# Optimization experiments

Measured on AMD Instinct MI355X. Metric: run time of the kernel, lower is better.

The kernel has to match this reference:

```python
import jax, jax.numpy as jnp
import numpy as np

N_NODES = 100000
N_EDGES = 1600000
D = 128  # num_node_features == hidden
N_LAYERS = 4


def setup_inputs() -> dict:
    key = jax.random.key(0)
    ks = jax.random.split(key, 6)
    x = jax.random.normal(ks[0], (N_NODES, D), dtype=jnp.float32)
    edge_index = jax.random.randint(ks[1], (2, N_EDGES), 0, N_NODES, dtype=jnp.int32)
    s = 1.0 / np.sqrt(D)
    Wl = jax.random.uniform(ks[2], (N_LAYERS, D, D), jnp.float32, -s, s)
    bl = jax.random.uniform(ks[3], (N_LAYERS, D), jnp.float32, -s, s)
    Wr = jax.random.uniform(ks[4], (N_LAYERS, D, D), jnp.float32, -s, s)
    return {"x": x, "edge_index": edge_index, "Wl": Wl, "bl": bl, "Wr": Wr}


def reference(x, edge_index, Wl, bl, Wr):
    src, dst = edge_index[0], edge_index[1]
    n = x.shape[0]
    # degree of each destination node (clamped to 1, matching scatter_mean)
    deg = jax.ops.segment_sum(jnp.ones_like(dst, dtype=x.dtype), dst, num_segments=n)
    inv_deg = (1.0 / jnp.maximum(deg, 1.0))[:, None]  # [N,1]
    for l in range(Wl.shape[0]):
        # mean-aggregate source features into destination nodes
        agg = jax.ops.segment_sum(x[src], dst, num_segments=n) * inv_deg  # [N,D]
        # SAGEConv: lin_l(agg) + lin_r(x)  (lin_r has no bias), then ReLU
        x = jax.nn.relu(agg @ Wl[l].T + bl[l] + x @ Wr[l].T)
    return x
```

## Files before the change

kernel.cpp:

```cpp
#include <hip/hip_runtime.h>
#include <hip/hip_fp16.h>

#define D 128
#define TM 32
#define AHP 264

typedef float f4v __attribute__((ext_vector_type(4)));
typedef float f2v __attribute__((ext_vector_type(2)));
typedef _Float16 h8v __attribute__((ext_vector_type(8)));

#define Q8_SCALE 16.0f
#define Q8_INV   0.0625f

static __device__ __forceinline__ unsigned pkh(float a, float b) {
    __half2 h = __float22half2_rn(make_float2(a, b));
    return *(unsigned*)&h;
}


__global__ void hist_kernel(const int* __restrict__ dst, int* __restrict__ deg, int E) {
    int i = blockIdx.x * blockDim.x + threadIdx.x;
    if (i < E) atomicAdd(&deg[dst[i]], 1);
}

__global__ void scan1_kernel(const int* __restrict__ deg, int* __restrict__ local_excl,
                             int* __restrict__ blocksum, int n) {
    __shared__ int tmp[1024];
    int i = blockIdx.x * 1024 + threadIdx.x;
    int v = (i < n) ? deg[i] : 0;
    tmp[threadIdx.x] = v;
    __syncthreads();
    for (int off = 1; off < 1024; off <<= 1) {
        int t = 0;
        if (threadIdx.x >= off) t = tmp[threadIdx.x - off];
        __syncthreads();
        if (threadIdx.x >= off) tmp[threadIdx.x] += t;
        __syncthreads();
    }
    int incl = tmp[threadIdx.x];
    if (i < n) local_excl[i] = incl - v;
    if (threadIdx.x == 1023) blocksum[blockIdx.x] = tmp[1023];
}

__global__ void scan2_kernel(int* __restrict__ blocksum, int nb) {
    __shared__ int tmp[1024];
    int v = (threadIdx.x < nb) ? blocksum[threadIdx.x] : 0;
    tmp[threadIdx.x] = v;
    __syncthreads();
    for (int off = 1; off < 1024; off <<= 1) {
        int t = 0;
        if (threadIdx.x >= off) t = tmp[threadIdx.x - off];
        __syncthreads();
        if (threadIdx.x >= off) tmp[threadIdx.x] += t;
        __syncthreads();
    }
    if (threadIdx.x < nb) blocksum[threadIdx.x] = tmp[threadIdx.x] - v;
}

__global__ void scan3_kernel(const int* __restrict__ deg, const int* __restrict__ local_excl,
                             const int* __restrict__ blocksum, int* __restrict__ row_start,
                             int* __restrict__ cursor, float* __restrict__ inv_deg,
                             int n, int n_edges) {
    int i = blockIdx.x * 1024 + threadIdx.x;
    if (i < n) {
        int rs = local_excl[i] + blocksum[blockIdx.x];
        row_start[i] = rs;
        cursor[i]    = rs;
        inv_deg[i]   = 1.0f / fmaxf((float)deg[i], 1.0f);
    }
    if (i == 0) row_start[n] = n_edges;
}

__global__ void scatter_kernel(const int* __restrict__ src, const int* __restrict__ dst,
                               int* __restrict__ cursor, int* __restrict__ csr,
                               int E, int npx) {
    int x  = blockIdx.x & 7;
    int lo = x * npx, hi = lo + npx;
    int stride = (gridDim.x >> 3) * blockDim.x;
    for (int i = (blockIdx.x >> 3) * blockDim.x + threadIdx.x; i < E; i += stride) {
        int d = dst[i];
        if (d >= lo && d < hi) {
            int p = atomicAdd(&cursor[d], 1);
            csr[p] = src[i] << 7;
        }
    }
}

__global__ void prepack_w(const float* __restrict__ Wl, const float* __restrict__ Wr,
                          __half* __restrict__ wpack, int total) {
    int t = blockIdx.x * blockDim.x + threadIdx.x;
    if (t >= total) return;
    int lane = t & 63;
    int ks   = (t >> 6) & 7;
    int ft   = (t >> 9) & 7;
    int l    = t >> 12;
    int f = ft * 16 + (lane & 15);
    int k = (ks & 3) * 32 + ((lane >> 4) << 3);
    const float* W = (ks < 4) ? Wl : Wr;
    const float* src = W + ((size_t)l << 14) + ((size_t)f << 7) + k;
    float4 v0 = *(const float4*)src;
    float4 v1 = *(const float4*)(src + 4);
    uint4 u = {pkh(v0.x, v0.y), pkh(v0.z, v0.w), pkh(v1.x, v1.y), pkh(v1.z, v1.w)};
    ((uint4*)wpack)[t] = u;
}


__global__ void x_to_fp8(const float* __restrict__ x, unsigned* __restrict__ xq, int total4) {
    int i = blockIdx.x * blockDim.x + threadIdx.x;
    if (i < total4) {
        float4 v = ((const float4*)x)[i];
        unsigned u = 0;
        u = __builtin_amdgcn_cvt_pk_fp8_f32(v.x * Q8_SCALE, v.y * Q8_SCALE, u, false);
        u = __builtin_amdgcn_cvt_pk_fp8_f32(v.z * Q8_SCALE, v.w * Q8_SCALE, u, true);
        xq[i] = u;
    }
}


#define ACC16Q(V) {                                                          \
    f2v a0_ = __builtin_amdgcn_cvt_pk_f32_fp8((int)(V).x, false);            \
    f2v a1_ = __builtin_amdgcn_cvt_pk_f32_fp8((int)(V).x, true);             \
    f2v b0_ = __builtin_amdgcn_cvt_pk_f32_fp8((int)(V).y, false);            \
    f2v b1_ = __builtin_amdgcn_cvt_pk_f32_fp8((int)(V).y, true);             \
    f2v c0_ = __builtin_amdgcn_cvt_pk_f32_fp8((int)(V).z, false);            \
    f2v c1_ = __builtin_amdgcn_cvt_pk_f32_fp8((int)(V).z, true);             \
    f2v d0_ = __builtin_amdgcn_cvt_pk_f32_fp8((int)(V).w, false);            \
    f2v d1_ = __builtin_amdgcn_cvt_pk_f32_fp8((int)(V).w, true);             \
    s0.x += a0_.x; s0.y += a0_.y; s0.z += a1_.x; s0.w += a1_.y;              \
    s1.x += b0_.x; s1.y += b0_.y; s1.z += b1_.x; s1.w += b1_.y;              \
    s2.x += c0_.x; s2.y += c0_.y; s2.z += c1_.x; s2.w += c1_.y;              \
    s3.x += d0_.x; s3.y += d0_.y; s3.z += d1_.x; s3.w += d1_.y; }

#define ACC8(V) { const __half2* hp_ = (const __half2*)&(V);                 \
    float2 f0_ = __half22float2(hp_[0]); float2 f1_ = __half22float2(hp_[1]);\
    float2 f2_ = __half22float2(hp_[2]); float2 f3_ = __half22float2(hp_[3]);\
    sA.x += f0_.x; sA.y += f0_.y; sA.z += f1_.x; sA.w += f1_.y;              \
    sB.x += f2_.x; sB.y += f2_.y; sB.z += f3_.x; sB.w += f3_.y; }

template<int INFMT, int OUTFMT>
__global__ __launch_bounds__(256, 4)
void sage_layer_mfma(const float* __restrict__ xin,
                     const void* __restrict__ xq_in,
                     float* __restrict__ xout,
                     void* __restrict__ xq_out,
                     const int* __restrict__ row_start, const int* __restrict__ csr,
                     const float* __restrict__ inv_deg,
                     const __half* __restrict__ wpack,
                     const float* __restrict__ bl, int n_nodes) {
    __shared__ __align__(16) __half Ah[TM][AHP];
    int block0 = blockIdx.x * TM;
    int tid = threadIdx.x;
    int lane = tid & 63;
    int wv   = tid >> 6;

    {
        int row = tid >> 3;
        int seg = tid & 7;
        int nn = block0 + row;
        f4v v0 = {0,0,0,0}, v1 = v0, v2 = v0, v3 = v0;
        if (nn < n_nodes) {
            const f4v* xp = (const f4v*)(xin + (size_t)nn * D) + seg * 4;
            v0 = __builtin_nontemporal_load(xp);
            v1 = __builtin_nontemporal_load(xp + 1);
            v2 = __builtin_nontemporal_load(xp + 2);
            v3 = __builtin_nontemporal_load(xp + 3);
        }
        uint4 ua = {pkh(v0.x,v0.y), pkh(v0.z,v0.w), pkh(v1.x,v1.y), pkh(v1.z,v1.w)};
        uint4 ub = {pkh(v2.x,v2.y), pkh(v2.z,v2.w), pkh(v3.x,v3.y), pkh(v3.z,v3.w)};
        uint4* dst = (uint4*)&Ah[row][128 + seg * 16];
        dst[0] = ua; dst[1] = ub;
    }

    if constexpr (INFMT == 0) {
        int g   = tid >> 3;
        int sub = tid & 7;
        int n = block0 + g;
        float4 s0 = {0,0,0,0}, s1 = {0,0,0,0}, s2 = {0,0,0,0}, s3 = {0,0,0,0};
        float idg = 1.f;
        int e0 = 0, e1 = 0;
        if (n < n_nodes) {
            e0 = row_start[n];
            e1 = row_start[n + 1];
            idg = inv_deg[n];
        }
        int e = e0;
        if (e < e1) {
            int last = e1 - 1;
            const char* qbase = (const char*)xq_in;
            int laneoff = sub * 16;
            int i0 = csr[min(e,     last)];
            int i1 = csr[min(e + 1, last)];
            int i2 = csr[min(e + 2, last)];
            int i3 = csr[min(e + 3, last)];
            while (1) {
                uint4 v0 = *(const uint4*)(qbase + (size_t)(i0 + laneoff));
                uint4 v1 = *(const uint4*)(qbase + (size_t)(i1 + laneoff));
                uint4 v2 = *(const uint4*)(qbase + (size_t)(i2 + laneoff));
                uint4 v3 = *(const uint4*)(qbase + (size_t)(i3 + laneoff));
                int en = e + 4;
                bool more = en < e1;
                int p0, p1, p2, p3;
                if (more) {
                    p0 = csr[min(en,     last)];
                    p1 = csr[min(en + 1, last)];
                    p2 = csr[min(en + 2, last)];
                    p3 = csr[min(en + 3, last)];
                }
                ACC16Q(v0)
                if (e + 1 <= last) ACC16Q(v1)
                if (e + 2 <= last) ACC16Q(v2)
                if (e + 3 <= last) ACC16Q(v3)
                if (!more) break;
                e = en;
                i0 = p0; i1 = p1; i2 = p2; i3 = p3;
            }
        }
        float sc = idg * Q8_INV;
        uint4 ua = {pkh(s0.x*sc,s0.y*sc), pkh(s0.z*sc,s0.w*sc),
                    pkh(s1.x*sc,s1.y*sc), pkh(s1.z*sc,s1.w*sc)};
        uint4 ub = {pkh(s2.x*sc,s2.y*sc), pkh(s2.z*sc,s2.w*sc),
                    pkh(s3.x*sc,s3.y*sc), pkh(s3.z*sc,s3.w*sc)};
        uint4* dst = (uint4*)&Ah[g][sub * 16];
        dst[0] = ua; dst[1] = ub;
    } else {
        int g   = tid >> 4;
        int sub = tid & 15;
        const char* hbase = (const char*)xq_in;
        int laneoff = sub * 16;
        for (int t = 0; t < 2; ++t) {
            int j = g + t * 16;
            int n = block0 + j;
            float4 sA = {0,0,0,0}, sB = {0,0,0,0};
            float idg = 1.f;
            int e0 = 0, e1 = 0;
            if (n < n_nodes) {
                e0 = row_start[n];
                e1 = row_start[n + 1];
                idg = inv_deg[n];
            }
            int e = e0;
            if (e < e1) {
                int last = e1 - 1;
                int i0 = csr[min(e,     last)] << 1;
                int i1 = csr[min(e + 1, last)] << 1;
                int i2 = csr[min(e + 2, last)] << 1;
                int i3 = csr[min(e + 3, last)] << 1;
                while (1) {
                    float4 v0 = *(const float4*)(hbase + (size_t)(i0 + laneoff));
                    float4 v1 = *(const float4*)(hbase + (size_t)(i1 + laneoff));
                    float4 v2 = *(const float4*)(hbase + (size_t)(i2 + laneoff));
                    float4 v3 = *(const float4*)(hbase + (size_t)(i3 + laneoff));
                    int en = e + 4;
                    bool more = en < e1;
                    int p0, p1, p2, p3;
                    if (more) {
                        p0 = csr[min(en,     last)] << 1;
                        p1 = csr[min(en + 1, last)] << 1;
                        p2 = csr[min(en + 2, last)] << 1;
                        p3 = csr[min(en + 3, last)] << 1;
                    }
                    ACC8(v0)
                    if (e + 1 <= last) ACC8(v1)
                    if (e + 2 <= last) ACC8(v2)
                    if (e + 3 <= last) ACC8(v3)
                    if (!more) break;
                    e = en;
                    i0 = p0; i1 = p1; i2 = p2; i3 = p3;
                }
            }
            uint4 u = {pkh(sA.x*idg, sA.y*idg), pkh(sA.z*idg, sA.w*idg),
                       pkh(sB.x*idg, sB.y*idg), pkh(sB.z*idg, sB.w*idg)};
            *(uint4*)&Ah[j][sub * 8] = u;
        }
    }

    uint4 wf[16];
    {
        const uint4* wp = (const uint4*)wpack;
        #pragma unroll
        for (int i = 0; i < 16; ++i) {
            int ft = wv * 2 + (i >> 3);
            int ks = i & 7;
            wf[i] = wp[(size_t)(ft * 8 + ks) * 64 + lane];
        }
    }

    __syncthreads();

    {
        f4v acc[2][2];
        #pragma unroll
        for (int ft = 0; ft < 2; ++ft) {
            int f0 = wv * 32 + ft * 16 + ((lane >> 4) << 2);
            f4v bv = *(const f4v*)(bl + f0);
            acc[ft][0] = bv;
            acc[ft][1] = bv;
        }
        #pragma unroll
        for (int ks = 0; ks < 8; ++ks) {
            int koff = ks * 32 + ((lane >> 4) << 3);
            h8v b0 = *(const h8v*)&Ah[lane & 15][koff];
            h8v b1 = *(const h8v*)&Ah[16 + (lane & 15)][koff];
            h8v a0 = *(const h8v*)&wf[ks];
            h8v a1 = *(const h8v*)&wf[8 + ks];
            acc[0][0] = __builtin_amdgcn_mfma_f32_16x16x32_f16(a0, b0, acc[0][0], 0, 0, 0);
            acc[0][1] = __builtin_amdgcn_mfma_f32_16x16x32_f16(a0, b1, acc[0][1], 0, 0, 0);
            acc[1][0] = __builtin_amdgcn_mfma_f32_16x16x32_f16(a1, b0, acc[1][0], 0, 0, 0);
            acc[1][1] = __builtin_amdgcn_mfma_f32_16x16x32_f16(a1, b1, acc[1][1], 0, 0, 0);
        }
        #pragma unroll
        for (int ft = 0; ft < 2; ++ft) {
            #pragma unroll
            for (int nt = 0; nt < 2; ++nt) {
                int node = block0 + nt * 16 + (lane & 15);
                int f0 = wv * 32 + ft * 16 + ((lane >> 4) << 2);
                f4v r = acc[ft][nt];
                r.x = fmaxf(r.x, 0.f); r.y = fmaxf(r.y, 0.f);
                r.z = fmaxf(r.z, 0.f); r.w = fmaxf(r.w, 0.f);
                if (node < n_nodes) {
                    __builtin_nontemporal_store(r, (f4v*)(xout + (size_t)node * D + f0));
                    if constexpr (OUTFMT == 0) {
                        unsigned u = 0;
                        u = __builtin_amdgcn_cvt_pk_fp8_f32(r.x * Q8_SCALE, r.y * Q8_SCALE, u, false);
                        u = __builtin_amdgcn_cvt_pk_fp8_f32(r.z * Q8_SCALE, r.w * Q8_SCALE, u, true);
                        ((unsigned*)xq_out)[(size_t)node * 32 + (f0 >> 2)] = u;
                    } else if constexpr (OUTFMT == 1) {
                        uint2 u = {pkh(r.x, r.y), pkh(r.z, r.w)};
                        ((uint2*)xq_out)[(size_t)node * 32 + (f0 >> 2)] = u;
                    }
                }
            }
        }
    }
}

extern "C" void kernel_launch(void* const* d_in, const int* in_sizes, int n_in,
                              void* d_out, int out_size, void* d_ws, size_t ws_size,
                              hipStream_t stream) {
    const float* x  = (const float*)d_in[0];
    const int*  edge = (const int*)d_in[1];
    const float* Wl = (const float*)d_in[2];
    const float* bl = (const float*)d_in[3];
    const float* Wr = (const float*)d_in[4];

    int N = in_sizes[0] / D;
    int E = in_sizes[1] / 2;
    int L = in_sizes[3] / D;
    const int* srcp = edge;
    const int* dstp = edge + E;

    char* w = (char*)d_ws;
    auto alloc = [&](size_t bytes) {
        char* p = w;
        w += (bytes + 255) & ~(size_t)255;
        return p;
    };
    int*   deg       = (int*)alloc((size_t)N * 4);
    int*   local_ex  = (int*)alloc((size_t)N * 4);
    int*   row_start = (int*)alloc((size_t)(N + 1) * 4);
    int*   cursor    = (int*)alloc((size_t)N * 4);
    int*   csr       = (int*)alloc((size_t)E * 4);
    float* invdeg    = (float*)alloc((size_t)N * 4);
    int*   blocksum  = (int*)alloc((size_t)1024 * 4);
    __half* wpack    = (__half*)alloc((size_t)L * 32768 * 2);
    float* buf0      = (float*)alloc((size_t)N * D * 4);
    unsigned* q0     = (unsigned*)alloc((size_t)N * D);
    void*  q1        = (void*)alloc((size_t)N * D * 2);

    int nb1 = (N + 1023) / 1024;
    hipMemsetAsync(deg, 0, (size_t)N * 4, stream);
    hist_kernel<<<(E + 255) / 256, 256, 0, stream>>>(dstp, deg, E);
    scan1_kernel<<<nb1, 1024, 0, stream>>>(deg, local_ex, blocksum, N);
    scan2_kernel<<<1, 1024, 0, stream>>>(blocksum, nb1);
    scan3_kernel<<<nb1, 1024, 0, stream>>>(deg, local_ex, blocksum, row_start,
                                           cursor, invdeg, N, E);
    int npx = (N + 7) / 8;
    scatter_kernel<<<2048, 256, 0, stream>>>(srcp, dstp, cursor, csr, E, npx);
    int tp = L * 4096;
    prepack_w<<<(tp + 255) / 256, 256, 0, stream>>>(Wl, Wr, wpack, tp);
    int t4 = N * (D / 4);
    x_to_fp8<<<(t4 + 255) / 256, 256, 0, stream>>>(x, q0, t4);

    float* out = (float*)d_out;
    int nbl = (N + TM - 1) / TM;

    sage_layer_mfma<0, 0><<<nbl, 256, 0, stream>>>(x, q0, buf0, q1, row_start, csr, invdeg,
                                                   wpack + 0 * 32768, bl + 0 * D, N);
    sage_layer_mfma<0, 0><<<nbl, 256, 0, stream>>>(buf0, q1, out, q0, row_start, csr, invdeg,
                                                   wpack + 1 * 32768, bl + 1 * D, N);
    sage_layer_mfma<0, 1><<<nbl, 256, 0, stream>>>(out, q0, buf0, q1, row_start, csr, invdeg,
                                                   wpack + 2 * 32768, bl + 2 * D, N);
    sage_layer_mfma<1, 2><<<nbl, 256, 0, stream>>>(buf0, q1, out, nullptr, row_start, csr, invdeg,
                                                   wpack + 3 * 32768, bl + 3 * D, N);
}
```

Baseline: 516.6 us.

## Keep fp16 shadow of node features instead of fp32 intermediates between layers

Intermediate layers now write only fp16 (and fp8 where needed) copies of the activations, dropping the full fp32 store. The self-term load reads fp16 directly, halving its bytes and removing the in-kernel pack. The final layer alone writes fp32 output. Launch bounds also rise to 8 blocks per SM, which may constrain registers and cause spills.

Result: slower. 545.2 us (+5.5%).

```diff
diff --git a/kernel.cpp b/kernel.cpp
--- a/kernel.cpp
+++ b/kernel.cpp
@@ -105,7 +105,8 @@
 }
 
 
-__global__ void x_to_fp8(const float* __restrict__ x, unsigned* __restrict__ xq, int total4) {
+__global__ void x_to_shadow(const float* __restrict__ x, unsigned* __restrict__ xq,
+                            uint2* __restrict__ xh, int total4) {
     int i = blockIdx.x * blockDim.x + threadIdx.x;
     if (i < total4) {
         float4 v = ((const float4*)x)[i];
@@ -113,6 +114,8 @@
         u = __builtin_amdgcn_cvt_pk_fp8_f32(v.x * Q8_SCALE, v.y * Q8_SCALE, u, false);
         u = __builtin_amdgcn_cvt_pk_fp8_f32(v.z * Q8_SCALE, v.w * Q8_SCALE, u, true);
         xq[i] = u;
+        uint2 h = {pkh(v.x, v.y), pkh(v.z, v.w)};
+        xh[i] = h;
     }
 }
 
@@ -138,11 +141,12 @@
     sB.x += f2_.x; sB.y += f2_.y; sB.z += f3_.x; sB.w += f3_.y; }
 
 template<int INFMT, int OUTFMT>
-__global__ __launch_bounds__(256, 4)
-void sage_layer_mfma(const float* __restrict__ xin,
+__global__ __launch_bounds__(256, 8)
+void sage_layer_mfma(const __half* __restrict__ xh_in,
                      const void* __restrict__ xq_in,
                      float* __restrict__ xout,
-                     void* __restrict__ xq_out,
+                     unsigned* __restrict__ q8_out,
+                     uint2* __restrict__ h16_out,
                      const int* __restrict__ row_start, const int* __restrict__ csr,
                      const float* __restrict__ inv_deg,
                      const __half* __restrict__ wpack,
@@ -157,18 +161,14 @@
         int row = tid >> 3;
         int seg = tid & 7;
         int nn = block0 + row;
-        f4v v0 = {0,0,0,0}, v1 = v0, v2 = v0, v3 = v0;
+        uint4 a = {0,0,0,0}, b = a;
         if (nn < n_nodes) {
-            const f4v* xp = (const f4v*)(xin + (size_t)nn * D) + seg * 4;
-            v0 = __builtin_nontemporal_load(xp);
-            v1 = __builtin_nontemporal_load(xp + 1);
-            v2 = __builtin_nontemporal_load(xp + 2);
-            v3 = __builtin_nontemporal_load(xp + 3);
-        }
-        uint4 ua = {pkh(v0.x,v0.y), pkh(v0.z,v0.w), pkh(v1.x,v1.y), pkh(v1.z,v1.w)};
-        uint4 ub = {pkh(v2.x,v2.y), pkh(v2.z,v2.w), pkh(v3.x,v3.y), pkh(v3.z,v3.w)};
+            const uint4* hp = (const uint4*)(xh_in + (size_t)nn * D) + seg * 2;
+            a = hp[0];
+            b = hp[1];
+        }
         uint4* dst = (uint4*)&Ah[row][128 + seg * 16];
-        dst[0] = ua; dst[1] = ub;
+        dst[0] = a; dst[1] = b;
     }
 
     if constexpr (INFMT == 0) {
@@ -318,15 +318,17 @@
                 r.x = fmaxf(r.x, 0.f); r.y = fmaxf(r.y, 0.f);
                 r.z = fmaxf(r.z, 0.f); r.w = fmaxf(r.w, 0.f);
                 if (node < n_nodes) {
-                    __builtin_nontemporal_store(r, (f4v*)(xout + (size_t)node * D + f0));
-                    if constexpr (OUTFMT == 0) {
-                        unsigned u = 0;
-                        u = __builtin_amdgcn_cvt_pk_fp8_f32(r.x * Q8_SCALE, r.y * Q8_SCALE, u, false);
-                        u = __builtin_amdgcn_cvt_pk_fp8_f32(r.z * Q8_SCALE, r.w * Q8_SCALE, u, true);
-                        ((unsigned*)xq_out)[(size_t)node * 32 + (f0 >> 2)] = u;
-                    } else if constexpr (OUTFMT == 1) {
-                        uint2 u = {pkh(r.x, r.y), pkh(r.z, r.w)};
-                        ((uint2*)xq_out)[(size_t)node * 32 + (f0 >> 2)] = u;
+                    if constexpr (OUTFMT == 2) {
+                        __builtin_nontemporal_store(r, (f4v*)(xout + (size_t)node * D + f0));
+                    } else {
+                        uint2 hu = {pkh(r.x, r.y), pkh(r.z, r.w)};
+                        h16_out[(size_t)node * 32 + (f0 >> 2)] = hu;
+                        if constexpr (OUTFMT == 0) {
+                            unsigned u = 0;
+                            u = __builtin_amdgcn_cvt_pk_fp8_f32(r.x * Q8_SCALE, r.y * Q8_SCALE, u, false);
+                            u = __builtin_amdgcn_cvt_pk_fp8_f32(r.z * Q8_SCALE, r.w * Q8_SCALE, u, true);
+                            q8_out[(size_t)node * 32 + (f0 >> 2)] = u;
+                        }
                     }
                 }
             }
@@ -363,9 +365,10 @@
     float* invdeg    = (float*)alloc((size_t)N * 4);
     int*   blocksum  = (int*)alloc((size_t)1024 * 4);
     __half* wpack    = (__half*)alloc((size_t)L * 32768 * 2);
-    float* buf0      = (float*)alloc((size_t)N * D * 4);
     unsigned* q0     = (unsigned*)alloc((size_t)N * D);
-    void*  q1        = (void*)alloc((size_t)N * D * 2);
+    unsigned* q1     = (unsigned*)alloc((size_t)N * D);
+    __half* h0       = (__half*)alloc((size_t)N * D * 2);
+    __half* h1       = (__half*)alloc((size_t)N * D * 2);
 
     int nb1 = (N + 1023) / 1024;
     hipMemsetAsync(deg, 0, (size_t)N * 4, stream);
@@ -379,17 +382,21 @@
     int tp = L * 4096;
     prepack_w<<<(tp + 255) / 256, 256, 0, stream>>>(Wl, Wr, wpack, tp);
     int t4 = N * (D / 4);
-    x_to_fp8<<<(t4 + 255) / 256, 256, 0, stream>>>(x, q0, t4);
+    x_to_shadow<<<(t4 + 255) / 256, 256, 0, stream>>>(x, q0, (uint2*)h0, t4);
 
     float* out = (float*)d_out;
     int nbl = (N + TM - 1) / TM;
 
-    sage_layer_mfma<0, 0><<<nbl, 256, 0, stream>>>(x, q0, buf0, q1, row_start, csr, invdeg,
+    sage_layer_mfma<0, 0><<<nbl, 256, 0, stream>>>(h0, q0, nullptr, q1, (uint2*)h1,
+                                                   row_start, csr, invdeg,
                                                    wpack + 0 * 32768, bl + 0 * D, N);
-    sage_layer_mfma<0, 0><<<nbl, 256, 0, stream>>>(buf0, q1, out, q0, row_start, csr, invdeg,
+    sage_layer_mfma<0, 0><<<nbl, 256, 0, stream>>>(h1, q1, nullptr, q0, (uint2*)h0,
+                                                   row_start, csr, invdeg,
                                                    wpack + 1 * 32768, bl + 1 * D, N);
-    sage_layer_mfma<0, 1><<<nbl, 256, 0, stream>>>(out, q0, buf0, q1, row_start, csr, invdeg,
+    sage_layer_mfma<0, 1><<<nbl, 256, 0, stream>>>(h0, q0, nullptr, nullptr, (uint2*)h1,
+                                                   row_start, csr, invdeg,
                                                    wpack + 2 * 32768, bl + 2 * D, N);
-    sage_layer_mfma<1, 2><<<nbl, 256, 0, stream>>>(buf0, q1, out, nullptr, row_start, csr, invdeg,
+    sage_layer_mfma<1, 2><<<nbl, 256, 0, stream>>>(h1, h1, out, nullptr, nullptr,
+                                                   row_start, csr, invdeg,
                                                    wpack + 3 * 32768, bl + 3 * D, N);
 }
```
